# Performance work log

Measured on AMD Instinct MI355X. Metric: run time of the kernel, lower is better.

Reference implementation:

```python
import jax, jax.numpy as jnp
import numpy as np

B, N, ADIM, VDIM = 16, 8192, 256, 128
KERN = 4  # edges_to_nodes conv kernel, padding=KERN//2 -> length E -> E+1 = N


def setup_inputs() -> dict:
    key = jax.random.key(0)
    ks = jax.random.split(key, 12)
    pos_0 = jax.random.normal(ks[0], (B, N, 3), dtype=jnp.float32)
    pos_1 = jax.random.normal(ks[1], (B, N, 3), dtype=jnp.float32)
    # VecLinear(4, vdim): W (vdim, 4), init std = fan_in**-0.5
    W_v = jax.random.normal(ks[2], (VDIM, 4), dtype=jnp.float32) * (4 ** -0.5)
    # scalar MLP: Linear(4, adim) -> LeakyReLU(0.2) -> Linear(adim, adim)
    W1 = jax.random.normal(ks[3], (ADIM, 4), dtype=jnp.float32) * (4 ** -0.5)
    b1 = jax.random.normal(ks[4], (ADIM,), dtype=jnp.float32) * 0.02
    W2 = jax.random.normal(ks[5], (ADIM, ADIM), dtype=jnp.float32) * (ADIM ** -0.5)
    b2 = jax.random.normal(ks[6], (ADIM,), dtype=jnp.float32) * 0.02
    # ScalConv1d(adim, 4, edges_to_nodes=True): Conv1d(adim, adim, 4, padding=2), with bias
    K_a = jax.random.normal(ks[7], (ADIM, ADIM, KERN), dtype=jnp.float32) * ((ADIM * KERN) ** -0.5)
    b_a = jax.random.normal(ks[8], (ADIM,), dtype=jnp.float32) * 0.02
    # VecConv1d(vdim, 4, edges_to_nodes=True): Conv1d(vdim, vdim, 4, padding=2), no bias
    K_v = jax.random.normal(ks[9], (VDIM, VDIM, KERN), dtype=jnp.float32) * ((VDIM * KERN) ** -0.5)
    return {"pos_0": pos_0, "pos_1": pos_1, "W_v": W_v, "W1": W1, "b1": b1,
            "W2": W2, "b2": b2, "K_a": K_a, "b_a": b_a, "K_v": K_v}


def _forward(pos_0, pos_1, W_v, W1, b1, W2, b2, K_a, b_a, K_v):
    batch = pos_0.shape[0]
    # relative displacement features on path edges: (B, E, 4, 3), E = N-1
    vecs = jnp.stack([
        pos_0[:, 1:] - pos_0[:, :-1],
        pos_1[:, 1:] - pos_1[:, :-1],
        pos_1[:, :-1] - pos_0[:, 1:],
        pos_1[:, 1:] - pos_0[:, :-1],
    ], axis=2)
    norms = jnp.sqrt(jnp.sum(vecs * vecs, axis=-1))  # (B, E, 4)
    # scalar MLP with LeakyReLU(0.2)
    h = jnp.einsum('bef,af->bea', norms, W1) + b1
    h = jnp.where(h >= 0, h, 0.2 * h)
    y_a = jnp.einsum('bea,oa->beo', h, W2) + b2          # (B, E, adim)
    # VecLinear: 'oi,...ik->...ok'
    y_v = jnp.einsum('oi,beik->beok', W_v, vecs)          # (B, E, vdim, 3)
    dn = ('NCH', 'OIH', 'NCH')
    # ScalConv1d edges_to_nodes: Conv1d(adim, adim, 4, padding=2) -> length E+1 = N
    xa = jnp.transpose(y_a, (0, 2, 1))                    # (B, adim, E)
    a = jax.lax.conv_general_dilated(xa, K_a, (1,), [(2, 2)], dimension_numbers=dn)
    a = a + b_a[None, :, None]
    a_out = jnp.transpose(a, (0, 2, 1))                   # (B, N, adim)
    # VecConv1d edges_to_nodes: fold 3 spatial components into batch, no bias
    xv = jnp.transpose(y_v, (0, 3, 2, 1)).reshape(3 * batch, VDIM, -1)  # (3B, vdim, E)
    v = jax.lax.conv_general_dilated(xv, K_v, (1,), [(2, 2)], dimension_numbers=dn)
    v_out = jnp.transpose(v.reshape(batch, 3, VDIM, -1), (0, 3, 2, 1))  # (B, N, vdim, 3)
    return a_out, v_out


def reference(pos_0, pos_1, W_v, W1, b1, W2, b2, K_a, b_a, K_v):
    return _forward(pos_0, pos_1, W_v, W1, b1, W2, b2, K_a, b_a, K_v)
```

## Files before the change

kernel.cpp:

```cpp
#include <hip/hip_runtime.h>
#include <stdint.h>

#define NN 8192
#define EE 8191
#define AD 256
#define BB 16

typedef unsigned short u16;
typedef short bf16x8 __attribute__((ext_vector_type(8)));
typedef float f32x4 __attribute__((ext_vector_type(4)));
typedef u16 u16x8 __attribute__((ext_vector_type(8)));

__device__ __forceinline__ u16 f2bf(float f) {
  unsigned u = __builtin_bit_cast(unsigned, f);
  u = u + 0x7fffu + ((u >> 16) & 1u);
  return (u16)(u >> 16);
}

__global__ __launch_bounds__(256) void prep_ma(const float* __restrict__ W2,
                                               const float* __restrict__ b2,
                                               const float* __restrict__ K_a,
                                               const float* __restrict__ b_a,
                                               const float* __restrict__ W_v,
                                               const float* __restrict__ K_v,
                                               u16* __restrict__ Ma,
                                               float* __restrict__ bk,
                                               float* __restrict__ bias_all,
                                               float* __restrict__ Mv) {
  __shared__ float ka[256][4];
  __shared__ float b2s[256];
  __shared__ float red[4];
  const int tid = threadIdx.x;
  const int o = blockIdx.x;
  const float4 kv = ((const float4*)K_a)[(size_t)o * 256 + tid];
  ka[tid][0] = kv.x; ka[tid][1] = kv.y; ka[tid][2] = kv.z; ka[tid][3] = kv.w;
  b2s[tid] = b2[tid];
  __syncthreads();
  float acc[4] = {0.f, 0.f, 0.f, 0.f};
  for (int c = 0; c < 256; ++c) {
    const float w = W2[(c << 8) + tid];
    acc[0] += ka[c][0] * w; acc[1] += ka[c][1] * w;
    acc[2] += ka[c][2] * w; acc[3] += ka[c][3] * w;
  }
  const int ac = tid >> 6, ks = (tid >> 5) & 1, jj = tid & 31;
#pragma unroll
  for (int t = 0; t < 4; ++t)
    Ma[((size_t)((t * 8 + ac * 2 + ks) * 256 + o)) * 32 + jj] = f2bf(acc[t]);
  if (tid < 4) {
    float s = 0.f;
    for (int c = 0; c < 256; ++c) s += ka[c][tid] * b2s[c];
    bk[tid * 256 + o] = s;
    red[tid] = s;
  }
  __syncthreads();
  if (tid == 0) bias_all[o] = b_a[o] + red[0] + red[1] + red[2] + red[3];
  if (blockIdx.x < 8) {
    const int idx2 = blockIdx.x * 256 + tid;
    const int k = idx2 >> 9, rem = idx2 & 511, ov = rem >> 2, i = rem & 3;
    float a2 = 0.f;
    for (int c = 0; c < 128; ++c)
      a2 += K_v[(size_t)((ov << 7) + c) * 4 + k] * W_v[(c << 2) + i];
    Mv[idx2] = a2;
  }
}

#define MM(Bf, Af, C) __builtin_amdgcn_mfma_f32_16x16x32_bf16((Bf), (Af), (C), 0, 0, 0)

__global__ __launch_bounds__(512, 2) void gemm_a(const float* __restrict__ p0,
                                                 const float* __restrict__ p1,
                                                 const float* __restrict__ W1,
                                                 const float* __restrict__ b1,
                                                 const u16* __restrict__ Ma,
                                                 const float* __restrict__ bias_all,
                                                 const float* __restrict__ bk,
                                                 float* __restrict__ out) {
  __shared__ __align__(16) char hs[259 * 528];
  __shared__ float nrm[259][4];
  const int tid = threadIdx.x;
  const int lane = tid & 63;
  const int wid = tid >> 6;
  const int wm = wid >> 2, wn = wid & 3;
  const int b = blockIdx.x >> 5;
  const int n0 = (blockIdx.x & 31) * 256;
  const int lhi = lane >> 4;
  const int llo = lane & 15;

  const size_t pbase = (size_t)b * NN * 3;
  for (int idx = tid; idx < 1036; idx += 512) {
    const int rr = idx >> 2, i = idx & 3;
    const int e = n0 + rr - 2;
    float v = 0.f;
    if (e >= 0 && e < EE) {
      const float* P0 = p0 + pbase;
      const float* P1 = p1 + pbase;
      const float* hi = (i == 0) ? P0 + (size_t)(e + 1) * 3
                      : (i == 1) ? P1 + (size_t)(e + 1) * 3
                      : (i == 2) ? P1 + (size_t)e * 3
                                 : P1 + (size_t)(e + 1) * 3;
      const float* lo = (i == 0) ? P0 + (size_t)e * 3
                      : (i == 1) ? P1 + (size_t)e * 3
                      : (i == 2) ? P0 + (size_t)(e + 1) * 3
                                 : P0 + (size_t)e * 3;
      const float dx = hi[0] - lo[0], dy = hi[1] - lo[1], dz = hi[2] - lo[2];
      v = sqrtf(dx * dx + dy * dy + dz * dz);
    }
    nrm[rr][i] = v;
  }
  __syncthreads();

  {
    const int g8 = tid & 31;
    const int strip = tid >> 5;
    float w1r[8][4], b1r[8];
    const float4* W14 = (const float4*)W1;
#pragma unroll
    for (int j = 0; j < 8; ++j) {
      const float4 w = W14[g8 * 8 + j];
      w1r[j][0] = w.x; w1r[j][1] = w.y; w1r[j][2] = w.z; w1r[j][3] = w.w;
      b1r[j] = b1[g8 * 8 + j];
    }
    for (int rr = strip; rr < 259; rr += 16) {
      const int e = n0 + rr - 2;
      const bool valid = (e >= 0) && (e < EE);
      const float nA = nrm[rr][0], nB = nrm[rr][1], nC = nrm[rr][2], nD = nrm[rr][3];
      u16x8 pack;
#pragma unroll
      for (int j = 0; j < 8; ++j) {
        float v = b1r[j] + nA * w1r[j][0] + nB * w1r[j][1] +
                  nC * w1r[j][2] + nD * w1r[j][3];
        v = (v >= 0.f) ? v : 0.2f * v;
        pack[j] = valid ? f2bf(v) : (u16)0;
      }
      *(u16x8*)(hs + rr * 528 + g8 * 16) = pack;
    }
  }
  __syncthreads();

  const f32x4 zero = {0.f, 0.f, 0.f, 0.f};
  f32x4 acc[8][4];
#pragma unroll
  for (int m = 0; m < 8; ++m)
#pragma unroll
    for (int nf = 0; nf < 4; ++nf) acc[m][nf] = zero;

  const char* mb = (const char*)Ma + (size_t)(wn * 64 + llo) * 64 + (size_t)lhi * 16;
  const char* ha = hs + (wm * 128 + llo) * 528;

  bf16x8 pA0, pA1, pA2, pA3, pB0, pB1, pB2, pB3;
  pA0 = *(const bf16x8*)(mb);
  pA1 = *(const bf16x8*)(mb + 1024);
  pA2 = *(const bf16x8*)(mb + 2048);
  pA3 = *(const bf16x8*)(mb + 3072);

#pragma unroll 1
  for (int s = 0; s < 32; s += 2) {
    {
      const char* bp = mb + (size_t)(s + 1) * 16384;
      pB0 = *(const bf16x8*)(bp);
      pB1 = *(const bf16x8*)(bp + 1024);
      pB2 = *(const bf16x8*)(bp + 2048);
      pB3 = *(const bf16x8*)(bp + 3072);
    }
    const int tap = s >> 3;
    const int cAe = ((s >> 1) & 3) * 128 + lhi * 16;
    {
      const int ro = tap * 528 + cAe;
#pragma unroll
      for (int m = 0; m < 8; ++m) {
        const bf16x8 af = *(const bf16x8*)(ha + m * 16 * 528 + ro);
        acc[m][0] = MM(pA0, af, acc[m][0]);
        acc[m][1] = MM(pA1, af, acc[m][1]);
        acc[m][2] = MM(pA2, af, acc[m][2]);
        acc[m][3] = MM(pA3, af, acc[m][3]);
      }
    }
    {
      const int sp = (s + 2 < 32) ? (s + 2) : 31;
      const char* bp = mb + (size_t)sp * 16384;
      pA0 = *(const bf16x8*)(bp);
      pA1 = *(const bf16x8*)(bp + 1024);
      pA2 = *(const bf16x8*)(bp + 2048);
      pA3 = *(const bf16x8*)(bp + 3072);
    }
    {
      const int ro = tap * 528 + cAe + 64;
#pragma unroll
      for (int m = 0; m < 8; ++m) {
        const bf16x8 af = *(const bf16x8*)(ha + m * 16 * 528 + ro);
        acc[m][0] = MM(pB0, af, acc[m][0]);
        acc[m][1] = MM(pB1, af, acc[m][1]);
        acc[m][2] = MM(pB2, af, acc[m][2]);
        acc[m][3] = MM(pB3, af, acc[m][3]);
      }
    }
  }

#pragma unroll
  for (int m = 0; m < 8; ++m) {
    const int node = n0 + wm * 128 + m * 16 + llo;
    float* orow = out + ((size_t)b * NN + node) * AD;
    const bool edge = (node <= 1) | (node >= NN - 2);
#pragma unroll
    for (int nf = 0; nf < 4; ++nf) {
      const int o0 = wn * 64 + nf * 16 + lhi * 4;
      float bx = bias_all[o0], by = bias_all[o0 + 1],
            bz = bias_all[o0 + 2], bw = bias_all[o0 + 3];
      if (edge) {
        const float* k0 = bk + o0;
        const float* k1 = bk + 256 + o0;
        const float* k2 = bk + 512 + o0;
        const float* k3 = bk + 768 + o0;
        if (node == 0) {
          bx -= k0[0] + k1[0]; by -= k0[1] + k1[1];
          bz -= k0[2] + k1[2]; bw -= k0[3] + k1[3];
        } else if (node == 1) {
          bx -= k0[0]; by -= k0[1]; bz -= k0[2]; bw -= k0[3];
        } else if (node == NN - 2) {
          bx -= k3[0]; by -= k3[1]; bz -= k3[2]; bw -= k3[3];
        } else {
          bx -= k2[0] + k3[0]; by -= k2[1] + k3[1];
          bz -= k2[2] + k3[2]; bw -= k2[3] + k3[3];
        }
      }
      float4 st;
      st.x = acc[m][nf][0] + bx;
      st.y = acc[m][nf][1] + by;
      st.z = acc[m][nf][2] + bz;
      st.w = acc[m][nf][3] + bw;
      *(float4*)(orow + o0) = st;
    }
  }
}

__global__ __launch_bounds__(256) void vec_path(const float* __restrict__ p0,
                                                const float* __restrict__ p1,
                                                const float* __restrict__ Mv,
                                                float* __restrict__ out) {
  __shared__ float MvS[2048];
  __shared__ __align__(16) float ob[32 * 384];
  const int tid = threadIdx.x;
  const int b = blockIdx.x >> 8;
  const int n0 = (blockIdx.x & 255) * 32;
  for (int idx = tid; idx < 2048; idx += 256) MvS[idx] = Mv[idx];
  __syncthreads();
  const int nl = tid >> 3, q = tid & 7;
  const int n = n0 + nl;
  const size_t pbase = (size_t)b * NN * 3;
  float s[4][4][3];
#pragma unroll
  for (int k = 0; k < 4; ++k) {
    const int e = n + k - 2;
    if (e >= 0 && e < EE) {
      const float* A0 = p0 + pbase + (size_t)e * 3;
      const float* A1 = p0 + pbase + (size_t)(e + 1) * 3;
      const float* C0 = p1 + pbase + (size_t)e * 3;
      const float* C1 = p1 + pbase + (size_t)(e + 1) * 3;
#pragma unroll
      for (int d = 0; d < 3; ++d) {
        const float a0v = A0[d], a1v = A1[d], c0v = C0[d], c1v = C1[d];
        s[k][0][d] = a1v - a0v;
        s[k][1][d] = c1v - c0v;
        s[k][2][d] = c0v - a1v;
        s[k][3][d] = c1v - a0v;
      }
    } else {
#pragma unroll
      for (int i2 = 0; i2 < 4; ++i2)
#pragma unroll
        for (int d = 0; d < 3; ++d) s[k][i2][d] = 0.f;
    }
  }
  for (int oi = 0; oi < 16; ++oi) {
    const int o = q * 16 + oi;
    float r0 = 0.f, r1 = 0.f, r2 = 0.f;
#pragma unroll
    for (int k = 0; k < 4; ++k) {
      const float* mp = &MvS[((k << 7) + o) << 2];
#pragma unroll
      for (int i2 = 0; i2 < 4; ++i2) {
        const float m = mp[i2];
        r0 += m * s[k][i2][0];
        r1 += m * s[k][i2][1];
        r2 += m * s[k][i2][2];
      }
    }
    ob[nl * 384 + o * 3 + 0] = r0;
    ob[nl * 384 + o * 3 + 1] = r1;
    ob[nl * 384 + o * 3 + 2] = r2;
  }
  __syncthreads();
  float4* dst = (float4*)(out + 33554432ULL + ((size_t)b * NN + n0) * 384);
  const float4* srcv = (const float4*)ob;
  for (int idx = tid; idx < 3072; idx += 256) dst[idx] = srcv[idx];
}

extern "C" void kernel_launch(void* const* d_in, const int* in_sizes, int n_in,
                              void* d_out, int out_size, void* d_ws, size_t ws_size,
                              hipStream_t stream) {
  const float* pos_0 = (const float*)d_in[0];
  const float* pos_1 = (const float*)d_in[1];
  const float* W_v = (const float*)d_in[2];
  const float* W1 = (const float*)d_in[3];
  const float* b1 = (const float*)d_in[4];
  const float* W2 = (const float*)d_in[5];
  const float* b2 = (const float*)d_in[6];
  const float* K_a = (const float*)d_in[7];
  const float* b_a = (const float*)d_in[8];
  const float* K_v = (const float*)d_in[9];
  float* out = (float*)d_out;
  char* ws = (char*)d_ws;

  const size_t MA_BYTES = (size_t)32 * 256 * 32 * 2;
  u16* Ma = (u16*)(ws);
  float* bk = (float*)(ws + MA_BYTES);
  float* bias_all = (float*)(ws + MA_BYTES + 4096);
  float* Mv = (float*)(ws + MA_BYTES + 4096 + 1024);

  prep_ma<<<dim3(256), dim3(256), 0, stream>>>(W2, b2, K_a, b_a, W_v, K_v,
                                               Ma, bk, bias_all, Mv);
  gemm_a<<<dim3(512), dim3(512), 0, stream>>>(pos_0, pos_1, W1, b1, Ma,
                                              bias_all, bk, out);
  vec_path<<<dim3(4096), dim3(256), 0, stream>>>(pos_0, pos_1, Mv, out);
}
```

Baseline: 207.9 us.

## Swizzle LDS activations, software-pipeline LDS fragment loads, and simplify vec_path

The hidden-activation tile in shared memory is now stored with an XOR-style column swizzle so the MFMA fragment reads hit different banks. The GEMM inner loop is restructured to prefetch activation fragments from LDS into registers one phase ahead, interleaving them with the MFMAs. Separately, vec_path is rewritten to use one thread per (node, output channel), with Mv held in registers and no LDS staging or block syncs. That version uses 16x more blocks and writes its output with strided scalar stores. The extra prefetch registers may raise register pressure in the GEMM.

```diff
diff --git a/kernel.cpp b/kernel.cpp
--- a/kernel.cpp
+++ b/kernel.cpp
@@ -131,7 +131,8 @@
         v = (v >= 0.f) ? v : 0.2f * v;
         pack[j] = valid ? f2bf(v) : (u16)0;
       }
-      *(u16x8*)(hs + rr * 528 + g8 * 16) = pack;
+      const int cs = (g8 & 24) | ((g8 + rr) & 7);
+      *(u16x8*)(hs + rr * 528 + (cs << 4)) = pack;
     }
   }
   __syncthreads();
@@ -144,7 +145,8 @@
     for (int nf = 0; nf < 4; ++nf) acc[m][nf] = zero;
 
   const char* mb = (const char*)Ma + (size_t)(wn * 64 + llo) * 64 + (size_t)lhi * 16;
-  const char* ha = hs + (wm * 128 + llo) * 528;
+  const int rb = wm * 128 + llo;
+  const int lt = llo + lhi;
 
   bf16x8 pA0, pA1, pA2, pA3, pB0, pB1, pB2, pB3;
   pA0 = *(const bf16x8*)(mb);
@@ -152,46 +154,91 @@
   pA2 = *(const bf16x8*)(mb + 2048);
   pA3 = *(const bf16x8*)(mb + 3072);
 
+  bf16x8 afA0, afA1, afA2, afA3, afB0, afB1, afB2, afB3;
+  {
+    const char* ap = hs + rb * 528 + (((lt) & 7) << 4);
+    afA0 = *(const bf16x8*)(ap);
+    afA1 = *(const bf16x8*)(ap + 8448);
+    afA2 = *(const bf16x8*)(ap + 16896);
+    afA3 = *(const bf16x8*)(ap + 25344);
+  }
+
 #pragma unroll 1
   for (int s = 0; s < 32; s += 2) {
+    const int tap = s >> 3;
+    const int q = (s >> 1) & 3;
+    const int swe = (lt + tap) & 7;
+    const char* rowp = hs + (rb + tap) * 528 + (q << 7);
+    const char* ape = rowp + (swe << 4);
+    const char* apo = rowp + ((swe ^ 4) << 4);
     {
       const char* bp = mb + (size_t)(s + 1) * 16384;
       pB0 = *(const bf16x8*)(bp);
       pB1 = *(const bf16x8*)(bp + 1024);
       pB2 = *(const bf16x8*)(bp + 2048);
       pB3 = *(const bf16x8*)(bp + 3072);
-    }
-    const int tap = s >> 3;
-    const int cAe = ((s >> 1) & 3) * 128 + lhi * 16;
+      afB0 = *(const bf16x8*)(ape + 33792);
+      afB1 = *(const bf16x8*)(ape + 42240);
+      afB2 = *(const bf16x8*)(ape + 50688);
+      afB3 = *(const bf16x8*)(ape + 59136);
+      acc[0][0] = MM(pA0, afA0, acc[0][0]); acc[1][0] = MM(pA0, afA1, acc[1][0]);
+      acc[2][0] = MM(pA0, afA2, acc[2][0]); acc[3][0] = MM(pA0, afA3, acc[3][0]);
+      acc[0][1] = MM(pA1, afA0, acc[0][1]); acc[1][1] = MM(pA1, afA1, acc[1][1]);
+      acc[2][1] = MM(pA1, afA2, acc[2][1]); acc[3][1] = MM(pA1, afA3, acc[3][1]);
+      acc[0][2] = MM(pA2, afA0, acc[0][2]); acc[1][2] = MM(pA2, afA1, acc[1][2]);
+      acc[2][2] = MM(pA2, afA2, acc[2][2]); acc[3][2] = MM(pA2, afA3, acc[3][2]);
+      acc[0][3] = MM(pA3, afA0, acc[0][3]); acc[1][3] = MM(pA3, afA1, acc[1][3]);
+      acc[2][3] = MM(pA3, afA2, acc[2][3]); acc[3][3] = MM(pA3, afA3, acc[3][3]);
+      afA0 = *(const bf16x8*)(apo);
+      afA1 = *(const bf16x8*)(apo + 8448);
+      afA2 = *(const bf16x8*)(apo + 16896);
+      afA3 = *(const bf16x8*)(apo + 25344);
+      acc[4][0] = MM(pA0, afB0, acc[4][0]); acc[5][0] = MM(pA0, afB1, acc[5][0]);
+      acc[6][0] = MM(pA0, afB2, acc[6][0]); acc[7][0] = MM(pA0, afB3, acc[7][0]);
+      acc[4][1] = MM(pA1, afB0, acc[4][1]); acc[5][1] = MM(pA1, afB1, acc[5][1]);
+      acc[6][1] = MM(pA1, afB2, acc[6][1]); acc[7][1] = MM(pA1, afB3, acc[7][1]);
+      acc[4][2] = MM(pA2, afB0, acc[4][2]); acc[5][2] = MM(pA2, afB1, acc[5][2]);
+      acc[6][2] = MM(pA2, afB2, acc[6][2]); acc[7][2] = MM(pA2, afB3, acc[7][2]);
+      acc[4][3] = MM(pA3, afB0, acc[4][3]); acc[5][3] = MM(pA3, afB1, acc[5][3]);
+      acc[6][3] = MM(pA3, afB2, acc[6][3]); acc[7][3] = MM(pA3, afB3, acc[7][3]);
+    }
     {
-      const int ro = tap * 528 + cAe;
-#pragma unroll
-      for (int m = 0; m < 8; ++m) {
-        const bf16x8 af = *(const bf16x8*)(ha + m * 16 * 528 + ro);
-        acc[m][0] = MM(pA0, af, acc[m][0]);
-        acc[m][1] = MM(pA1, af, acc[m][1]);
-        acc[m][2] = MM(pA2, af, acc[m][2]);
-        acc[m][3] = MM(pA3, af, acc[m][3]);
-      }
-    }
-    {
-      const int sp = (s + 2 < 32) ? (s + 2) : 31;
-      const char* bp = mb + (size_t)sp * 16384;
+      const int s2 = (s + 2) & 31;
+      const char* bp = mb + (size_t)s2 * 16384;
       pA0 = *(const bf16x8*)(bp);
       pA1 = *(const bf16x8*)(bp + 1024);
       pA2 = *(const bf16x8*)(bp + 2048);
       pA3 = *(const bf16x8*)(bp + 3072);
-    }
-    {
-      const int ro = tap * 528 + cAe + 64;
-#pragma unroll
-      for (int m = 0; m < 8; ++m) {
-        const bf16x8 af = *(const bf16x8*)(ha + m * 16 * 528 + ro);
-        acc[m][0] = MM(pB0, af, acc[m][0]);
-        acc[m][1] = MM(pB1, af, acc[m][1]);
-        acc[m][2] = MM(pB2, af, acc[m][2]);
-        acc[m][3] = MM(pB3, af, acc[m][3]);
+      afB0 = *(const bf16x8*)(apo + 33792);
+      afB1 = *(const bf16x8*)(apo + 42240);
+      afB2 = *(const bf16x8*)(apo + 50688);
+      afB3 = *(const bf16x8*)(apo + 59136);
+      acc[0][0] = MM(pB0, afA0, acc[0][0]); acc[1][0] = MM(pB0, afA1, acc[1][0]);
+      acc[2][0] = MM(pB0, afA2, acc[2][0]); acc[3][0] = MM(pB0, afA3, acc[3][0]);
+      acc[0][1] = MM(pB1, afA0, acc[0][1]); acc[1][1] = MM(pB1, afA1, acc[1][1]);
+      acc[2][1] = MM(pB1, afA2, acc[2][1]); acc[3][1] = MM(pB1, afA3, acc[3][1]);
+      acc[0][2] = MM(pB2, afA0, acc[0][2]); acc[1][2] = MM(pB2, afA1, acc[1][2]);
+      acc[2][2] = MM(pB2, afA2, acc[2][2]); acc[3][2] = MM(pB2, afA3, acc[3][2]);
+      acc[0][3] = MM(pB3, afA0, acc[0][3]); acc[1][3] = MM(pB3, afA1, acc[1][3]);
+      acc[2][3] = MM(pB3, afA2, acc[2][3]); acc[3][3] = MM(pB3, afA3, acc[3][3]);
+      {
+        const int tap2 = s2 >> 3;
+        const int q2 = (s2 >> 1) & 3;
+        const char* ap2 = hs + (rb + tap2) * 528 + (q2 << 7) +
+                          ((((lt + tap2) & 7)) << 4);
+        afA0 = *(const bf16x8*)(ap2);
+        afA1 = *(const bf16x8*)(ap2 + 8448);
+        afA2 = *(const bf16x8*)(ap2 + 16896);
+        afA3 = *(const bf16x8*)(ap2 + 25344);
       }
+      acc[4][0] = MM(pB0, afB0, acc[4][0]); acc[5][0] = MM(pB0, afB1, acc[5][0]);
+      acc[6][0] = MM(pB0, afB2, acc[6][0]); acc[7][0] = MM(pB0, afB3, acc[7][0]);
+      acc[4][1] = MM(pB1, afB0, acc[4][1]); acc[5][1] = MM(pB1, afB1, acc[5][1]);
+      acc[6][1] = MM(pB1, afB2, acc[6][1]); acc[7][1] = MM(pB1, afB3, acc[7][1]);
+      acc[4][2] = MM(pB2, afB0, acc[4][2]); acc[5][2] = MM(pB2, afB1, acc[5][2]);
+      acc[6][2] = MM(pB2, afB2, acc[6][2]); acc[7][2] = MM(pB2, afB3, acc[7][2]);
+      acc[4][3] = MM(pB3, afB0, acc[4][3]); acc[5][3] = MM(pB3, afB1, acc[5][3]);
+      acc[6][3] = MM(pB3, afB2, acc[6][3]); acc[7][3] = MM(pB3, afB3, acc[7][3]);
     }
   }
 
@@ -236,62 +283,49 @@
                                                 const float* __restrict__ p1,
                                                 const float* __restrict__ Mv,
                                                 float* __restrict__ out) {
-  __shared__ float MvS[2048];
-  __shared__ __align__(16) float ob[32 * 384];
   const int tid = threadIdx.x;
-  const int b = blockIdx.x >> 8;
-  const int n0 = (blockIdx.x & 255) * 32;
-  for (int idx = tid; idx < 2048; idx += 256) MvS[idx] = Mv[idx];
-  __syncthreads();
-  const int nl = tid >> 3, q = tid & 7;
-  const int n = n0 + nl;
-  const size_t pbase = (size_t)b * NN * 3;
-  float s[4][4][3];
+  const int nl = tid >> 7, o = tid & 127;
+  const int b = blockIdx.x >> 12;
+  const int n = ((blockIdx.x & 4095) << 1) + nl;
+  const float4* Mv4 = (const float4*)Mv;
+  float mv[4][4];
+#pragma unroll
+  for (int k = 0; k < 4; ++k) {
+    const float4 v = Mv4[k * 128 + o];
+    mv[k][0] = v.x; mv[k][1] = v.y; mv[k][2] = v.z; mv[k][3] = v.w;
+  }
+  const size_t pb = (size_t)b * NN * 3;
+  float q0[5][3], q1[5][3];
+#pragma unroll
+  for (int j = 0; j < 5; ++j) {
+    int pos = n - 2 + j;
+    pos = pos < 0 ? 0 : (pos > NN - 1 ? NN - 1 : pos);
+    const float* a = p0 + pb + (size_t)pos * 3;
+    const float* c = p1 + pb + (size_t)pos * 3;
+    q0[j][0] = a[0]; q0[j][1] = a[1]; q0[j][2] = a[2];
+    q1[j][0] = c[0]; q1[j][1] = c[1]; q1[j][2] = c[2];
+  }
+  float r0 = 0.f, r1 = 0.f, r2 = 0.f;
 #pragma unroll
   for (int k = 0; k < 4; ++k) {
     const int e = n + k - 2;
-    if (e >= 0 && e < EE) {
-      const float* A0 = p0 + pbase + (size_t)e * 3;
-      const float* A1 = p0 + pbase + (size_t)(e + 1) * 3;
-      const float* C0 = p1 + pbase + (size_t)e * 3;
-      const float* C1 = p1 + pbase + (size_t)(e + 1) * 3;
-#pragma unroll
-      for (int d = 0; d < 3; ++d) {
-        const float a0v = A0[d], a1v = A1[d], c0v = C0[d], c1v = C1[d];
-        s[k][0][d] = a1v - a0v;
-        s[k][1][d] = c1v - c0v;
-        s[k][2][d] = c0v - a1v;
-        s[k][3][d] = c1v - a0v;
-      }
-    } else {
-#pragma unroll
-      for (int i2 = 0; i2 < 4; ++i2)
-#pragma unroll
-        for (int d = 0; d < 3; ++d) s[k][i2][d] = 0.f;
-    }
-  }
-  for (int oi = 0; oi < 16; ++oi) {
-    const int o = q * 16 + oi;
-    float r0 = 0.f, r1 = 0.f, r2 = 0.f;
-#pragma unroll
-    for (int k = 0; k < 4; ++k) {
-      const float* mp = &MvS[((k << 7) + o) << 2];
-#pragma unroll
-      for (int i2 = 0; i2 < 4; ++i2) {
-        const float m = mp[i2];
-        r0 += m * s[k][i2][0];
-        r1 += m * s[k][i2][1];
-        r2 += m * s[k][i2][2];
-      }
-    }
-    ob[nl * 384 + o * 3 + 0] = r0;
-    ob[nl * 384 + o * 3 + 1] = r1;
-    ob[nl * 384 + o * 3 + 2] = r2;
-  }
-  __syncthreads();
-  float4* dst = (float4*)(out + 33554432ULL + ((size_t)b * NN + n0) * 384);
-  const float4* srcv = (const float4*)ob;
-  for (int idx = tid; idx < 3072; idx += 256) dst[idx] = srcv[idx];
+    const float vs = (e >= 0 && e < EE) ? 1.f : 0.f;
+    const float c0 = mv[k][0] * vs, c1 = mv[k][1] * vs,
+                c2 = mv[k][2] * vs, c3 = mv[k][3] * vs;
+#pragma unroll
+    for (int d = 0; d < 3; ++d) {
+      const float a0 = q0[k][d], a1 = q0[k + 1][d];
+      const float p0v = q1[k][d], p1v = q1[k + 1][d];
+      const float v0 = a1 - a0;
+      const float v1 = p1v - p0v;
+      const float v2 = p0v - a1;
+      const float v3 = p1v - a0;
+      const float rr = c0 * v0 + c1 * v1 + c2 * v2 + c3 * v3;
+      if (d == 0) r0 += rr; else if (d == 1) r1 += rr; else r2 += rr;
+    }
+  }
+  float* dst = out + 33554432ULL + (((size_t)b * NN + n) * 128 + o) * 3;
+  dst[0] = r0; dst[1] = r1; dst[2] = r2;
 }
 
 extern "C" void kernel_launch(void* const* d_in, const int* in_sizes, int n_in,
@@ -320,5 +354,5 @@
                                                Ma, bk, bias_all, Mv);
   gemm_a<<<dim3(512), dim3(512), 0, stream>>>(pos_0, pos_1, W1, b1, Ma,
                                               bias_all, bk, out);
-  vec_path<<<dim3(4096), dim3(256), 0, stream>>>(pos_0, pos_1, Mv, out);
-}
+  vec_path<<<dim3(65536), dim3(256), 0, stream>>>(pos_0, pos_1, Mv, out);
+}
```

Result: slower. 218.5 us (+5.1%).
